# Optimization experiments

Measured on AMD Instinct MI355X. Metric: run time of the kernel, lower is better.

Reference implementation:

```python
import jax, jax.numpy as jnp
import numpy as np

L, H, NH, F, S_MAX, VOCAB, STAR_V, OFF = 12, 768, 12, 3072, 512, 31090, 390, 30700
EPS = 1e-12

def _ln(x, g, b):
    m = x.mean(-1, keepdims=True)
    v = ((x - m) ** 2).mean(-1, keepdims=True)
    return (x - m) * jax.lax.rsqrt(v + EPS) * g + b

def setup_inputs() -> dict:
    key = jax.random.key(0)
    ks = iter(jax.random.split(key, 48))
    B, S = 16, 512
    p = lambda *s: jax.random.normal(next(ks), s, dtype=jnp.float32) * 0.02
    return dict(
        input_ids=jax.random.randint(next(ks), (B, S), 0, VOCAB),
        attention_mask=jnp.ones((B, S), dtype=jnp.int32),
        token_type_ids=jnp.zeros((B, S), dtype=jnp.int32),
        word_emb=p(VOCAB, H), star_emb=p(STAR_V, H),
        pos_emb=p(S_MAX, H), type_emb=p(2, H),
        emb_g=jnp.ones(H), emb_b=jnp.zeros(H),
        Wq=p(L, H, H), bq=jnp.zeros((L, H)), Wk=p(L, H, H), bk=jnp.zeros((L, H)),
        Wv=p(L, H, H), bv=jnp.zeros((L, H)), Wo=p(L, H, H), bo=jnp.zeros((L, H)),
        g1=jnp.ones((L, H)), b1=jnp.zeros((L, H)),
        Wi=p(L, H, F), bi=jnp.zeros((L, F)), Wf=p(L, F, H), bf=jnp.zeros((L, H)),
        g2=jnp.ones((L, H)), b2=jnp.zeros((L, H)),
        pool_W=p(H, H), pool_b=jnp.zeros(H))

def reference(input_ids, attention_mask, token_type_ids, word_emb, star_emb,
              pos_emb, type_emb, emb_g, emb_b, Wq, bq, Wk, bk, Wv, bv, Wo, bo,
              g1, b1, Wi, bi, Wf, bf, g2, b2, pool_W, pool_b):
    B, S = input_ids.shape
    dh = H // NH
    # vectorized masked embedding swap (replaces the per-token Python loop)
    star = input_ids >= OFF
    embs = jnp.where(star[..., None],
                     star_emb[jnp.clip(input_ids - OFF, 0, STAR_V - 1)],
                     word_emb[jnp.clip(input_ids, 0, VOCAB - 1)])
    x = _ln(embs + pos_emb[:S][None] + type_emb[token_type_ids], emb_g, emb_b)
    ext = (1.0 - attention_mask.astype(x.dtype))[:, None, None, :] * -10000.0
    scale = 1.0 / np.sqrt(dh).astype(np.float32)

    def layer(x, pr):
        wq, bq_, wk, bk_, wv, bv_, wo, bo_, g1_, b1_, wi, bi_, wf, bf_, g2_, b2_ = pr
        sp = lambda t: t.reshape(B, S, NH, dh).transpose(0, 2, 1, 3)  # [B,NH,S,dh]
        q, k, v = sp(x @ wq + bq_), sp(x @ wk + bk_), sp(x @ wv + bv_)
        att = jax.nn.softmax(jnp.einsum('bhqd,bhkd->bhqk', q, k) * scale + ext, axis=-1)
        ctx = jnp.einsum('bhqk,bhkd->bhqd', att, v).transpose(0, 2, 1, 3).reshape(B, S, H)
        x = _ln(x + ctx @ wo + bo_, g1_, b1_)
        x = _ln(x + jax.nn.gelu(x @ wi + bi_, approximate=False) @ wf + bf_, g2_, b2_)
        return x, None

    x, _ = jax.lax.scan(layer, x, (Wq, bq, Wk, bk, Wv, bv, Wo, bo,
                                   g1, b1, Wi, bi, Wf, bf, g2, b2))
    pooled = jnp.tanh(x[:, 0] @ pool_W + pool_b)
    return x, pooled
```

## Files before the change

kernel.cpp:

```cpp
#include <hip/hip_runtime.h>
#include <hip/hip_bf16.h>
#include <math.h>


#define L_   12
#define H_   768
#define NH_  12
#define DH_  64
#define F_   3072
#define B_   16
#define S_   512
#define NTOK (B_ * S_)
#define QKVN 2304

typedef __attribute__((ext_vector_type(8))) __bf16 bf16x8;
typedef __attribute__((ext_vector_type(4))) __bf16 bf16x4;
typedef __attribute__((ext_vector_type(4))) float  f32x4;

static __device__ __forceinline__ f32x4 mfma16(bf16x8 a, bf16x8 b, f32x4 c) {
  return __builtin_amdgcn_mfma_f32_16x16x32_bf16(a, b, c, 0, 0, 0);
}

static __device__ __forceinline__ void load_lds16(const void* g, void* l) {
  __builtin_amdgcn_global_load_lds(
      (const __attribute__((address_space(1))) void*)g,
      (__attribute__((address_space(3))) void*)l, 16, 0, 0);
}

static __device__ __forceinline__ float gelu_fast(float v) {
  const float u = 1.5957691216057308f * v * (1.0f + 0.044715f * v * v);
  return v / (1.0f + __expf(-u));
}

__global__ __launch_bounds__(256) void transpose_k(const float* __restrict__ in,
                                                   __bf16* __restrict__ out,
                                                   int R, int C, size_t outZ) {
  __shared__ float t[32][33];
  const int z = blockIdx.z;
  const float* inz = in + (size_t)z * R * C;
  __bf16* outz = out + (size_t)z * outZ;
  const int c0 = blockIdx.x * 32, r0 = blockIdx.y * 32;
  const int tx = threadIdx.x, ty = threadIdx.y;
#pragma unroll
  for (int i = 0; i < 32; i += 8)
    t[ty + i][tx] = inz[(size_t)(r0 + ty + i) * C + c0 + tx];
  __syncthreads();
#pragma unroll
  for (int i = 0; i < 32; i += 8)
    outz[(size_t)(c0 + ty + i) * R + r0 + tx] = (__bf16)t[tx][ty + i];
}

__global__ __launch_bounds__(256) void concat_bias(const float* __restrict__ bq,
                                                   const float* __restrict__ bk,
                                                   const float* __restrict__ bv,
                                                   float* __restrict__ o) {
  const int i = blockIdx.x * 256 + threadIdx.x;
  if (i >= L_ * QKVN) return;
  const int l = i / QKVN, j = i - l * QKVN;
  float v;
  if (j < H_) v = bq[l * H_ + j];
  else if (j < 2 * H_) v = bk[l * H_ + j - H_];
  else v = bv[l * H_ + j - 2 * H_];
  o[i] = v;
}

template <int EPI, int OUTBF, int VT>
__global__ __launch_bounds__(256, 3) void gemm_n64(const __bf16* __restrict__ A,
                                                   const __bf16* __restrict__ Bt,
                                                   const float* __restrict__ bias,
                                                   float* __restrict__ Cf,
                                                   __bf16* __restrict__ Cb,
                                                   __bf16* __restrict__ vtp,
                                                   int M, int N, int K, int Ntiles) {
  alignas(16) __shared__ __bf16 lds[24576];
  const int tid = threadIdx.x, wid = tid >> 6, lane = tid & 63;
  int bid = blockIdx.x;
  const int nwg = gridDim.x;
  if ((nwg & 7) == 0) bid = (bid & 7) * (nwg >> 3) + (bid >> 3);
  const int bm = (bid / Ntiles) << 7, bn = (bid % Ntiles) << 6;
  const int nt = K >> 6;

  const __bf16* pA[4];
  const __bf16* pB[2];
#pragma unroll
  for (int j = 0; j < 4; ++j) {
    const int E = (j << 11) + tid * 8;
    const int Ep = E ^ (((E >> 8) & 1) << 4);
    const int r = ((Ep >> 10) << 4) | ((Ep >> 5) & 15);
    const int c = (((Ep >> 9) & 1) << 5) | (Ep & 31);
    pA[j] = A + (size_t)(bm + r) * K + c;
    if (j < 2) pB[j] = Bt + (size_t)(bn + r) * K + c;
  }

  auto stage = [&](int t, int buf) {
    __bf16* base = &lds[buf * 12288 + (wid << 9)];
    const size_t off = (size_t)(t << 6);
#pragma unroll
    for (int j = 0; j < 4; ++j) load_lds16(pA[j] + off, base + (j << 11));
#pragma unroll
    for (int j = 0; j < 2; ++j) load_lds16(pB[j] + off, base + 8192 + (j << 11));
  };

  const int frow = lane & 15, fk = (lane >> 4) << 3;
  const int swzb = (frow * 32 + fk) ^ (((frow >> 3) & 1) << 4);
  const int mh = wid >> 1, nq = wid & 1;

  f32x4 acc[4][2] = {};

  stage(0, 0);
  asm volatile("s_waitcnt vmcnt(0)" ::: "memory");
  __builtin_amdgcn_s_barrier();

  for (int t = 0; t < nt; ++t) {
    const int buf = t & 1;
    if (t + 1 < nt) stage(t + 1, buf ^ 1);
    const __bf16* LA = &lds[buf * 12288 + (mh << 12)];
    const __bf16* LB = &lds[buf * 12288 + 8192 + (nq << 11)];
    bf16x8 a[4][2], b[2][2];
#pragma unroll
    for (int mi = 0; mi < 4; ++mi)
#pragma unroll
      for (int ks = 0; ks < 2; ++ks)
        a[mi][ks] = *(const bf16x8*)&LA[mi * 1024 + ks * 512 + swzb];
#pragma unroll
    for (int ni = 0; ni < 2; ++ni)
#pragma unroll
      for (int ks = 0; ks < 2; ++ks)
        b[ni][ks] = *(const bf16x8*)&LB[ni * 1024 + ks * 512 + swzb];
    asm volatile("s_waitcnt lgkmcnt(0)" ::: "memory");
    __builtin_amdgcn_s_setprio(1);
#pragma unroll
    for (int mi = 0; mi < 4; ++mi)
#pragma unroll
      for (int ni = 0; ni < 2; ++ni)
#pragma unroll
        for (int ks = 0; ks < 2; ++ks)
          acc[mi][ni] = mfma16(a[mi][ks], b[ni][ks], acc[mi][ni]);
    __builtin_amdgcn_s_setprio(0);
    asm volatile("s_waitcnt vmcnt(0)" ::: "memory");
    __builtin_amdgcn_s_barrier();
  }

  const int r0 = (lane >> 4) << 2, c0 = lane & 15;
  const int wrow = bm + (mh << 6), wcol = bn + (nq << 5);
#pragma unroll
  for (int ni = 0; ni < 2; ++ni) {
    const int col = wcol + (ni << 4) + c0;
    const float bv = bias[col];
    if (VT && (wcol + (ni << 4)) >= 2 * H_) {
      const int hh = (col - 2 * H_) >> 6, dd = (col - 2 * H_) & 63;
#pragma unroll
      for (int mi = 0; mi < 4; ++mi) {
        const int row = wrow + (mi << 4) + r0;
        bf16x4 pv;
#pragma unroll
        for (int r = 0; r < 4; ++r) pv[r] = (__bf16)(acc[mi][ni][r] + bv);
        const int bb2 = row >> 9, ss = row & 511;
        *(bf16x4*)&vtp[((size_t)(bb2 * NH_ + hh) * DH_ + dd) * S_ + ss] = pv;
      }
    } else {
#pragma unroll
      for (int mi = 0; mi < 4; ++mi) {
        const int row = wrow + (mi << 4) + r0;
#pragma unroll
        for (int r = 0; r < 4; ++r) {
          float v = acc[mi][ni][r] + bv;
          if (EPI == 1) v = gelu_fast(v);
          if (OUTBF)
            Cb[(size_t)(row + r) * N + col] = (__bf16)v;
          else
            Cf[(size_t)(row + r) * N + col] = v;
        }
      }
    }
  }
}

__global__ __launch_bounds__(256, 3) void attn_kernel(const __bf16* __restrict__ qkv,
                                                      const __bf16* __restrict__ vt,
                                                      const int* __restrict__ amask,
                                                      __bf16* __restrict__ ctx) {
  __shared__ float extm[S_];
  __shared__ __bf16 Pl[4][2][16][40];
  const int h = blockIdx.x, b = blockIdx.y, z = blockIdx.z;
  const int tid = threadIdx.x, wid = tid >> 6, lane = tid & 63;
  const size_t rowb = (size_t)b * S_ * QKVN + (size_t)h * DH_;
  const __bf16* vbase = vt + ((size_t)(b * NH_ + h) * DH_) * S_;

  for (int i = tid; i < S_; i += 256)
    extm[i] = (1.0f - (float)amask[b * S_ + i]) * -10000.0f;
  __syncthreads();

  const int c0 = lane & 15, g4 = lane >> 4;
  const int qt0 = z * 8 + wid * 2;
  bf16x8 qf[2][2];
#pragma unroll
  for (int qi = 0; qi < 2; ++qi) {
    const __bf16* qrow = qkv + rowb +
        (size_t)((qt0 + qi) * 16 + c0) * QKVN + (g4 << 3);
    qf[qi][0] = *(const bf16x8*)qrow;
    qf[qi][1] = *(const bf16x8*)(qrow + 32);
  }
  f32x4 oacc[2][4] = {};
  float mrow[2] = {-1e30f, -1e30f}, lsum[2] = {0.f, 0.f};

  bf16x8 kfr[2][2][2];
  bf16x8 vfr[2][4];
#pragma unroll
  for (int f = 0; f < 2; ++f) {
    const __bf16* krow = qkv + rowb + (size_t)(f * 16 + c0) * QKVN + H_ + (g4 << 3);
    kfr[0][f][0] = *(const bf16x8*)krow;
    kfr[0][f][1] = *(const bf16x8*)(krow + 32);
  }
#pragma unroll
  for (int dt = 0; dt < 4; ++dt)
    vfr[0][dt] = *(const bf16x8*)&vbase[(size_t)(dt * 16 + c0) * S_ + (g4 << 3)];

#pragma unroll
  for (int kt = 0; kt < 16; ++kt) {
    const int buf = kt & 1;
    if (kt + 1 < 16) {
#pragma unroll
      for (int f = 0; f < 2; ++f) {
        const __bf16* krow = qkv + rowb +
            (size_t)((kt + 1) * 32 + f * 16 + c0) * QKVN + H_ + (g4 << 3);
        kfr[buf ^ 1][f][0] = *(const bf16x8*)krow;
        kfr[buf ^ 1][f][1] = *(const bf16x8*)(krow + 32);
      }
#pragma unroll
      for (int dt = 0; dt < 4; ++dt)
        vfr[buf ^ 1][dt] = *(const bf16x8*)&vbase[(size_t)(dt * 16 + c0) * S_ +
                                                  (kt + 1) * 32 + (g4 << 3)];
    }
#pragma unroll
    for (int qi = 0; qi < 2; ++qi) {
      f32x4 sc[2];
      __builtin_amdgcn_s_setprio(1);
#pragma unroll
      for (int f = 0; f < 2; ++f) {
        f32x4 z2 = {};
        z2 = mfma16(kfr[buf][f][0], qf[qi][0], z2);
        z2 = mfma16(kfr[buf][f][1], qf[qi][1], z2);
#pragma unroll
        for (int r = 0; r < 4; ++r)
          sc[f][r] = z2[r] * 0.125f + extm[kt * 32 + f * 16 + (g4 << 2) + r];
      }
      __builtin_amdgcn_s_setprio(0);
      float mx = fmaxf(fmaxf(fmaxf(sc[0][0], sc[0][1]), fmaxf(sc[0][2], sc[0][3])),
                       fmaxf(fmaxf(sc[1][0], sc[1][1]), fmaxf(sc[1][2], sc[1][3])));
      mx = fmaxf(mx, __shfl_xor(mx, 16, 64));
      mx = fmaxf(mx, __shfl_xor(mx, 32, 64));
      const float mn = fmaxf(mrow[qi], mx);
      const float al = __expf(mrow[qi] - mn);
      mrow[qi] = mn;
      float rs = 0.f;
#pragma unroll
      for (int f = 0; f < 2; ++f)
#pragma unroll
        for (int r = 0; r < 4; ++r) {
          const float p = __expf(sc[f][r] - mn);
          sc[f][r] = p;
          rs += p;
        }
      rs += __shfl_xor(rs, 16, 64);
      rs += __shfl_xor(rs, 32, 64);
      lsum[qi] = lsum[qi] * al + rs;
#pragma unroll
      for (int f = 0; f < 2; ++f)
#pragma unroll
        for (int r = 0; r < 4; ++r)
          Pl[wid][qi][c0][f * 16 + (g4 << 2) + r] = (__bf16)sc[f][r];
      float alr[4];
#pragma unroll
      for (int r = 0; r < 4; ++r)
        alr[r] = __shfl(al, (lane & 48) | ((g4 << 2) + r), 64);
#pragma unroll
      for (int dt = 0; dt < 4; ++dt)
#pragma unroll
        for (int r = 0; r < 4; ++r) oacc[qi][dt][r] *= alr[r];
      const bf16x8 pa = *(const bf16x8*)&Pl[wid][qi][c0][g4 << 3];
      __builtin_amdgcn_s_setprio(1);
#pragma unroll
      for (int dt = 0; dt < 4; ++dt)
        oacc[qi][dt] = mfma16(pa, vfr[buf][dt], oacc[qi][dt]);
      __builtin_amdgcn_s_setprio(0);
    }
  }
#pragma unroll
  for (int qi = 0; qi < 2; ++qi) {
    float inv[4];
#pragma unroll
    for (int r = 0; r < 4; ++r)
      inv[r] = 1.0f / __shfl(lsum[qi], (lane & 48) | ((g4 << 2) + r), 64);
#pragma unroll
    for (int dt = 0; dt < 4; ++dt)
#pragma unroll
      for (int r = 0; r < 4; ++r)
        ctx[(size_t)b * S_ * H_ + (size_t)h * DH_ +
            (size_t)((qt0 + qi) * 16 + (g4 << 2) + r) * H_ + dt * 16 + c0] =
            (__bf16)(oacc[qi][dt][r] * inv[r]);
  }
}

__global__ __launch_bounds__(256) void addln_kernel(float* __restrict__ x,
                                                    const __bf16* __restrict__ t,
                                                    const float* __restrict__ g,
                                                    const float* __restrict__ bb,
                                                    __bf16* __restrict__ xb) {
  const int tok = blockIdx.x * 4 + (threadIdx.x >> 6);
  const int lane = threadIdx.x & 63;
  float* xr = x + (size_t)tok * H_;
  const __bf16* tr = t + (size_t)tok * H_;
  f32x4 v[3];
  float s = 0.f, s2 = 0.f;
#pragma unroll
  for (int i = 0; i < 3; ++i) {
    const int off = lane * 4 + i * 256;
    f32x4 a = *(const f32x4*)&xr[off];
    bf16x4 tb = *(const bf16x4*)&tr[off];
#pragma unroll
    for (int r = 0; r < 4; ++r) {
      v[i][r] = a[r] + (float)tb[r];
      s += v[i][r];
      s2 += v[i][r] * v[i][r];
    }
  }
#pragma unroll
  for (int o = 32; o > 0; o >>= 1) {
    s += __shfl_xor(s, o, 64);
    s2 += __shfl_xor(s2, o, 64);
  }
  const float mean = s * (1.0f / 768.0f);
  const float var = s2 * (1.0f / 768.0f) - mean * mean;
  const float rstd = rsqrtf(var + 1e-12f);
  __bf16* xbr = xb + (size_t)tok * H_;
#pragma unroll
  for (int i = 0; i < 3; ++i) {
    const int off = lane * 4 + i * 256;
    f32x4 gv = *(const f32x4*)&g[off];
    f32x4 bv = *(const f32x4*)&bb[off];
    f32x4 y;
    bf16x4 yb;
#pragma unroll
    for (int r = 0; r < 4; ++r) {
      y[r] = (v[i][r] - mean) * rstd * gv[r] + bv[r];
      yb[r] = (__bf16)y[r];
    }
    *(f32x4*)&xr[off] = y;
    *(bf16x4*)&xbr[off] = yb;
  }
}

__global__ __launch_bounds__(256) void embed_kernel(
    const int* __restrict__ ids, const int* __restrict__ tt,
    const float* __restrict__ we, const float* __restrict__ se,
    const float* __restrict__ pe, const float* __restrict__ te,
    const float* __restrict__ g, const float* __restrict__ bb,
    float* __restrict__ x, __bf16* __restrict__ xb) {
  const int tok = blockIdx.x, tid = threadIdx.x;
  const int sp = tok & (S_ - 1);
  const int id = ids[tok];
  const float* e = (id >= 30700) ? se + (size_t)(id - 30700) * H_
                                 : we + (size_t)id * H_;
  const float* pr = pe + (size_t)sp * H_;
  const float* ty = te + (size_t)tt[tok] * H_;
  float v0 = e[tid] + pr[tid] + ty[tid];
  float v1 = e[tid + 256] + pr[tid + 256] + ty[tid + 256];
  float v2 = e[tid + 512] + pr[tid + 512] + ty[tid + 512];
  float s = v0 + v1 + v2;
  float s2 = v0 * v0 + v1 * v1 + v2 * v2;
  __shared__ float red1[4], red2[4];
#pragma unroll
  for (int o = 32; o > 0; o >>= 1) {
    s += __shfl_xor(s, o, 64);
    s2 += __shfl_xor(s2, o, 64);
  }
  if ((tid & 63) == 0) { red1[tid >> 6] = s; red2[tid >> 6] = s2; }
  __syncthreads();
  s = red1[0] + red1[1] + red1[2] + red1[3];
  s2 = red2[0] + red2[1] + red2[2] + red2[3];
  const float mean = s * (1.0f / 768.0f);
  const float var = s2 * (1.0f / 768.0f) - mean * mean;
  const float rstd = rsqrtf(var + 1e-12f);
  float* xr = x + (size_t)tok * H_;
  __bf16* xbr = xb + (size_t)tok * H_;
  const float y0 = (v0 - mean) * rstd * g[tid] + bb[tid];
  const float y1 = (v1 - mean) * rstd * g[tid + 256] + bb[tid + 256];
  const float y2 = (v2 - mean) * rstd * g[tid + 512] + bb[tid + 512];
  xr[tid] = y0; xr[tid + 256] = y1; xr[tid + 512] = y2;
  xbr[tid] = (__bf16)y0; xbr[tid + 256] = (__bf16)y1; xbr[tid + 512] = (__bf16)y2;
}

__global__ __launch_bounds__(256) void pool_kernel(const float* __restrict__ x,
                                                   const __bf16* __restrict__ wT,
                                                   const float* __restrict__ pb,
                                                   float* __restrict__ out) {
  const int b = blockIdx.x, tid = threadIdx.x;
  __shared__ float xr[H_];
  for (int i = tid; i < H_; i += 256) xr[i] = x[(size_t)b * S_ * H_ + i];
  __syncthreads();
  for (int n = tid; n < H_; n += 256) {
    const __bf16* w = wT + (size_t)n * H_;
    float acc = 0.f;
    for (int k = 0; k < H_; ++k) acc += xr[k] * (float)w[k];
    out[(size_t)b * H_ + n] = tanhf(acc + pb[n]);
  }
}

extern "C" void kernel_launch(void* const* d_in, const int* in_sizes, int n_in,
                              void* d_out, int out_size, void* d_ws,
                              size_t ws_size, hipStream_t stream) {
  (void)in_sizes; (void)n_in; (void)out_size;
  const int* ids = (const int*)d_in[0];
  const int* am = (const int*)d_in[1];
  const int* tt = (const int*)d_in[2];
  const float* we = (const float*)d_in[3];
  const float* se = (const float*)d_in[4];
  const float* pe = (const float*)d_in[5];
  const float* te = (const float*)d_in[6];
  const float* eg = (const float*)d_in[7];
  const float* ebb = (const float*)d_in[8];
  const float* Wq = (const float*)d_in[9];
  const float* bq = (const float*)d_in[10];
  const float* Wk = (const float*)d_in[11];
  const float* bk = (const float*)d_in[12];
  const float* Wv = (const float*)d_in[13];
  const float* bv = (const float*)d_in[14];
  const float* Wo = (const float*)d_in[15];
  const float* bo = (const float*)d_in[16];
  const float* g1 = (const float*)d_in[17];
  const float* b1 = (const float*)d_in[18];
  const float* Wi = (const float*)d_in[19];
  const float* bi = (const float*)d_in[20];
  const float* Wf = (const float*)d_in[21];
  const float* bf_ = (const float*)d_in[22];
  const float* g2 = (const float*)d_in[23];
  const float* b2 = (const float*)d_in[24];
  const float* pw = (const float*)d_in[25];
  const float* pb = (const float*)d_in[26];

  const size_t WQKV = (size_t)L_ * QKVN * H_;
  const size_t WSQ = (size_t)L_ * H_ * H_;
  const size_t WSF = (size_t)L_ * H_ * F_;
  const size_t MN = (size_t)NTOK * H_;
  __bf16* wqkv = (__bf16*)d_ws;
  __bf16* wTo_ = wqkv + WQKV;
  __bf16* wTi_ = wTo_ + WSQ;
  __bf16* wTf_ = wTi_ + WSF;
  __bf16* wTp_ = wTf_ + WSF;
  __bf16* xb = wTp_ + (size_t)H_ * H_;
  __bf16* qkvb = xb + MN;
  __bf16* cb = qkvb + (size_t)NTOK * QKVN;
  __bf16* mid = cb + MN;
  __bf16* vtb = mid + (size_t)NTOK * F_;
  __bf16* t0b = vtb + MN;
  float* bqkv = (float*)(t0b + MN);
  const size_t needed = (size_t)((char*)(bqkv + (size_t)L_ * QKVN) - (char*)d_ws);
  if (ws_size < needed) return;

  float* x = (float*)d_out;
  float* pooled = x + MN;

  const dim3 tb(32, 8);
  const size_t zq = (size_t)QKVN * H_;
  transpose_k<<<dim3(24, 24, 12), tb, 0, stream>>>(Wq, wqkv, H_, H_, zq);
  transpose_k<<<dim3(24, 24, 12), tb, 0, stream>>>(Wk, wqkv + (size_t)H_ * H_, H_, H_, zq);
  transpose_k<<<dim3(24, 24, 12), tb, 0, stream>>>(Wv, wqkv + 2 * (size_t)H_ * H_, H_, H_, zq);
  transpose_k<<<dim3(24, 24, 12), tb, 0, stream>>>(Wo, wTo_, H_, H_, (size_t)H_ * H_);
  transpose_k<<<dim3(96, 24, 12), tb, 0, stream>>>(Wi, wTi_, H_, F_, (size_t)H_ * F_);
  transpose_k<<<dim3(24, 96, 12), tb, 0, stream>>>(Wf, wTf_, F_, H_, (size_t)H_ * F_);
  transpose_k<<<dim3(24, 24, 1), tb, 0, stream>>>(pw, wTp_, H_, H_, (size_t)H_ * H_);
  concat_bias<<<(L_ * QKVN + 255) / 256, 256, 0, stream>>>(bq, bk, bv, bqkv);

  embed_kernel<<<NTOK, 256, 0, stream>>>(ids, tt, we, se, pe, te, eg, ebb, x, xb);

  for (int l = 0; l < L_; ++l) {
    gemm_n64<0, 1, 1><<<(NTOK / 128) * (QKVN / 64), 256, 0, stream>>>(
        xb, wqkv + (size_t)l * QKVN * H_, bqkv + (size_t)l * QKVN,
        nullptr, qkvb, vtb, NTOK, QKVN, H_, QKVN / 64);

    attn_kernel<<<dim3(NH_, B_, 4), 256, 0, stream>>>(qkvb, vtb, am, cb);

    gemm_n64<0, 1, 0><<<(NTOK / 128) * (H_ / 64), 256, 0, stream>>>(
        cb, wTo_ + (size_t)l * H_ * H_, bo + l * H_, nullptr, t0b, nullptr,
        NTOK, H_, H_, H_ / 64);
    addln_kernel<<<NTOK / 4, 256, 0, stream>>>(x, t0b, g1 + l * H_, b1 + l * H_, xb);

    gemm_n64<1, 1, 0><<<(NTOK / 128) * (F_ / 64), 256, 0, stream>>>(
        xb, wTi_ + (size_t)l * H_ * F_, bi + l * F_, nullptr, mid, nullptr,
        NTOK, F_, H_, F_ / 64);
    gemm_n64<0, 1, 0><<<(NTOK / 128) * (H_ / 64), 256, 0, stream>>>(
        mid, wTf_ + (size_t)l * F_ * H_, bf_ + l * H_, nullptr, t0b, nullptr,
        NTOK, H_, F_, H_ / 64);
    addln_kernel<<<NTOK / 4, 256, 0, stream>>>(x, t0b, g2 + l * H_, b2 + l * H_, xb);
  }

  pool_kernel<<<B_, 256, 0, stream>>>(x, wTp_, pb, pooled);
}
```

Measured before the change: 3.282 ms.

## Stage attention K/V tiles through swizzled LDS with direct global-to-LDS loads

Each attention block now cooperatively loads K and V tiles into double-buffered, XOR-swizzled shared memory using global_load_lds, instead of every wave fetching its own fragments from global memory into registers. The four waves share one copy of each K/V tile, which cuts redundant global traffic and frees registers. The cost is a block-wide barrier per key tile and explicit waitcnt handling. Separately, the softmax probabilities are written to LDS as packed bf16x4 vectors rather than one scalar store each.

```diff
diff --git a/kernel.cpp b/kernel.cpp
--- a/kernel.cpp
+++ b/kernel.cpp
@@ -181,6 +181,8 @@
                                                       const int* __restrict__ amask,
                                                       __bf16* __restrict__ ctx) {
   __shared__ float extm[S_];
+  alignas(16) __shared__ __bf16 Kl[2][2048];
+  alignas(16) __shared__ __bf16 Vl[2][2048];
   __shared__ __bf16 Pl[4][2][16][40];
   const int h = blockIdx.x, b = blockIdx.y, z = blockIdx.z;
   const int tid = threadIdx.x, wid = tid >> 6, lane = tid & 63;
@@ -189,9 +191,23 @@
 
   for (int i = tid; i < S_; i += 256)
     extm[i] = (1.0f - (float)amask[b * S_ + i]) * -10000.0f;
-  __syncthreads();
+
+  const int E = tid * 8;
+  const int Ep = E ^ (((E >> 8) & 1) << 4);
+  const int krow = ((Ep >> 10) << 4) | ((Ep >> 5) & 15);
+  const int kcol = (((Ep >> 9) & 1) << 5) | (Ep & 31);
+  const __bf16* ksrc = qkv + rowb + (size_t)krow * QKVN + H_ + kcol;
+  const int vd = ((Ep >> 9) << 4) | ((Ep >> 5) & 15);
+  const int vs = Ep & 31;
+  const __bf16* vsrc = vbase + (size_t)vd * S_ + vs;
+
+  auto stageKV = [&](int kt, int buf) {
+    load_lds16(ksrc + (size_t)(kt * 32) * QKVN, &Kl[buf][E]);
+    load_lds16(vsrc + kt * 32, &Vl[buf][E]);
+  };
 
   const int c0 = lane & 15, g4 = lane >> 4;
+  const int swzb = (c0 * 32 + (g4 << 3)) ^ (((c0 >> 3) & 1) << 4);
   const int qt0 = z * 8 + wid * 2;
   bf16x8 qf[2][2];
 #pragma unroll
@@ -204,34 +220,24 @@
   f32x4 oacc[2][4] = {};
   float mrow[2] = {-1e30f, -1e30f}, lsum[2] = {0.f, 0.f};
 
-  bf16x8 kfr[2][2][2];
-  bf16x8 vfr[2][4];
-#pragma unroll
-  for (int f = 0; f < 2; ++f) {
-    const __bf16* krow = qkv + rowb + (size_t)(f * 16 + c0) * QKVN + H_ + (g4 << 3);
-    kfr[0][f][0] = *(const bf16x8*)krow;
-    kfr[0][f][1] = *(const bf16x8*)(krow + 32);
-  }
-#pragma unroll
-  for (int dt = 0; dt < 4; ++dt)
-    vfr[0][dt] = *(const bf16x8*)&vbase[(size_t)(dt * 16 + c0) * S_ + (g4 << 3)];
+  stageKV(0, 0);
+  asm volatile("s_waitcnt vmcnt(0)" ::: "memory");
+  __syncthreads();
 
 #pragma unroll
   for (int kt = 0; kt < 16; ++kt) {
     const int buf = kt & 1;
-    if (kt + 1 < 16) {
-#pragma unroll
-      for (int f = 0; f < 2; ++f) {
-        const __bf16* krow = qkv + rowb +
-            (size_t)((kt + 1) * 32 + f * 16 + c0) * QKVN + H_ + (g4 << 3);
-        kfr[buf ^ 1][f][0] = *(const bf16x8*)krow;
-        kfr[buf ^ 1][f][1] = *(const bf16x8*)(krow + 32);
-      }
-#pragma unroll
-      for (int dt = 0; dt < 4; ++dt)
-        vfr[buf ^ 1][dt] = *(const bf16x8*)&vbase[(size_t)(dt * 16 + c0) * S_ +
-                                                  (kt + 1) * 32 + (g4 << 3)];
-    }
+    if (kt + 1 < 16) stageKV(kt + 1, buf ^ 1);
+    bf16x8 kf[2][2], vf[4];
+#pragma unroll
+    for (int f = 0; f < 2; ++f)
+#pragma unroll
+      for (int half = 0; half < 2; ++half)
+        kf[f][half] = *(const bf16x8*)&Kl[buf][f * 1024 + half * 512 + swzb];
+#pragma unroll
+    for (int dt = 0; dt < 4; ++dt)
+      vf[dt] = *(const bf16x8*)&Vl[buf][dt * 512 + swzb];
+    asm volatile("s_waitcnt lgkmcnt(0)" ::: "memory");
 #pragma unroll
     for (int qi = 0; qi < 2; ++qi) {
       f32x4 sc[2];
@@ -239,8 +245,8 @@
 #pragma unroll
       for (int f = 0; f < 2; ++f) {
         f32x4 z2 = {};
-        z2 = mfma16(kfr[buf][f][0], qf[qi][0], z2);
-        z2 = mfma16(kfr[buf][f][1], qf[qi][1], z2);
+        z2 = mfma16(kf[f][0], qf[qi][0], z2);
+        z2 = mfma16(kf[f][1], qf[qi][1], z2);
 #pragma unroll
         for (int r = 0; r < 4; ++r)
           sc[f][r] = z2[r] * 0.125f + extm[kt * 32 + f * 16 + (g4 << 2) + r];
@@ -254,22 +260,20 @@
       const float al = __expf(mrow[qi] - mn);
       mrow[qi] = mn;
       float rs = 0.f;
-#pragma unroll
-      for (int f = 0; f < 2; ++f)
-#pragma unroll
-        for (int r = 0; r < 4; ++r) {
-          const float p = __expf(sc[f][r] - mn);
-          sc[f][r] = p;
-          rs += p;
-        }
+      bf16x4 p0, p1;
+#pragma unroll
+      for (int r = 0; r < 4; ++r) {
+        const float pa0 = __expf(sc[0][r] - mn);
+        const float pa1 = __expf(sc[1][r] - mn);
+        p0[r] = (__bf16)pa0;
+        p1[r] = (__bf16)pa1;
+        rs += pa0 + pa1;
+      }
       rs += __shfl_xor(rs, 16, 64);
       rs += __shfl_xor(rs, 32, 64);
       lsum[qi] = lsum[qi] * al + rs;
-#pragma unroll
-      for (int f = 0; f < 2; ++f)
-#pragma unroll
-        for (int r = 0; r < 4; ++r)
-          Pl[wid][qi][c0][f * 16 + (g4 << 2) + r] = (__bf16)sc[f][r];
+      *(bf16x4*)&Pl[wid][qi][c0][(g4 << 2)] = p0;
+      *(bf16x4*)&Pl[wid][qi][c0][16 + (g4 << 2)] = p1;
       float alr[4];
 #pragma unroll
       for (int r = 0; r < 4; ++r)
@@ -282,9 +286,11 @@
       __builtin_amdgcn_s_setprio(1);
 #pragma unroll
       for (int dt = 0; dt < 4; ++dt)
-        oacc[qi][dt] = mfma16(pa, vfr[buf][dt], oacc[qi][dt]);
+        oacc[qi][dt] = mfma16(pa, vf[dt], oacc[qi][dt]);
       __builtin_amdgcn_s_setprio(0);
     }
+    asm volatile("s_waitcnt vmcnt(0)" ::: "memory");
+    __builtin_amdgcn_s_barrier();
   }
 #pragma unroll
   for (int qi = 0; qi < 2; ++qi) {
```

After: 3.036 ms. 7.5% less time.
